# Performance work log

Measured on AMD Instinct MI355X. Metric: run time of the kernel, lower is better.

Reference implementation:

```python
import jax, jax.numpy as jnp
import numpy as np

K = 10
EPS = 1e-5

def leaky(x):
    return jnp.where(x >= 0, x, 0.2 * x)

def graph_feature(x, k):
    # x: (B, C, N) -> edge features (B, 2C, N, k), standard DGCNN get_graph_feature
    B, C, N = x.shape
    xx = jnp.sum(x * x, axis=1)                      # (B, N)
    inner = jnp.einsum('bcn,bcm->bnm', x, x)          # (B, N, N)
    pair = 2.0 * inner - xx[:, :, None] - xx[:, None, :]  # -||xi - xj||^2
    _, idx = jax.lax.top_k(pair, k)                   # (B, N, k)
    xt = jnp.transpose(x, (0, 2, 1))                  # (B, N, C)
    nbr = xt[jnp.arange(B)[:, None, None], idx]       # (B, N, k, C) gather
    ctr = jnp.broadcast_to(xt[:, :, None, :], nbr.shape)
    feat = jnp.concatenate([nbr - ctr, ctr], axis=-1)  # (B, N, k, 2C)
    return jnp.transpose(feat, (0, 3, 1, 2))          # (B, 2C, N, k)

def edge_block(x, W, k):
    # gather -> 1x1 conv (edge MLP) -> leaky relu -> max over neighbors
    e = graph_feature(x, k)                           # (B, 2C, N, k)
    h = leaky(jnp.einsum('oc,bcnk->bonk', W, e))      # (B, O, N, k)
    return jnp.max(h, axis=-1)                        # (B, O, N)

def bn(x, g, b, m, v):
    # inference batchnorm over channel axis 1; x: (B, C, ...) 
    shape = (1, -1) + (1,) * (x.ndim - 2)
    return (x - m.reshape(shape)) * (g.reshape(shape) * jax.lax.rsqrt(v.reshape(shape) + EPS)) + b.reshape(shape)

def setup_inputs() -> dict:
    key = jax.random.key(0)
    ks = jax.random.split(key, 20)
    s = lambda i, shape, scale: (jax.random.normal(ks[i], shape, jnp.float32) * scale)
    inp = {
        'input': jax.random.normal(ks[0], (759, 220, 3), jnp.float32),
        'W1': s(1, (32, 6), 0.4),
        'W2': s(2, (32, 64), 0.15),
        'W3': s(3, (64, 64), 0.15),
        'W4': s(4, (128, 128), 0.1),
        'W5': s(5, (512, 256), 0.08),
        'g5': 1.0 + s(6, (512,), 0.05), 'b5': s(7, (512,), 0.05),
        'm5': s(8, (512,), 0.05), 'v5': 1.0 + 0.1 * jax.random.uniform(ks[9], (512,), jnp.float32),
        'Wl1': s(10, (1024, 1024), 0.03),
        'g6': 1.0 + s(11, (1024,), 0.05), 'b6': s(12, (1024,), 0.05),
        'm6': s(13, (1024,), 0.05), 'v6': 1.0 + 0.1 * jax.random.uniform(ks[14], (1024,), jnp.float32),
        'Wl2': s(15, (380, 1024), 0.03),
        'bl2': s(16, (380,), 0.02),
    }
    return inp

def reference(input, W1, W2, W3, W4, W5, g5, b5, m5, v5, Wl1, g6, b6, m6, v6, Wl2, bl2):
    x = jnp.transpose(input.reshape(-1, 220, 3), (0, 2, 1))  # (B, 3, N)
    x1 = edge_block(x, W1, K)    # (B, 32, N)
    x2 = edge_block(x1, W2, K)   # (B, 32, N)
    x3 = edge_block(x2, W3, K)   # (B, 64, N)
    x4 = edge_block(x3, W4, K)   # (B, 128, N)
    xc = jnp.concatenate([x1, x2, x3, x4], axis=1)           # (B, 256, N)
    h = leaky(bn(jnp.einsum('oc,bcn->bon', W5, xc), g5, b5, m5, v5))  # (B, 512, N)
    p = jnp.concatenate([jnp.max(h, axis=-1), jnp.mean(h, axis=-1)], axis=1)  # (B, 1024)
    z = leaky(bn(p @ Wl1.T, g6, b6, m6, v6))  # dropout is identity in eval
    return z @ Wl2.T + bl2                     # (B, 380)
```

## Files before the change

### kernel.cpp

```cpp
#include <hip/hip_runtime.h>
#include <math.h>

#define NB 759
#define NPT 220
#define KNN 10
#define XCCH 256
#define LDXC (XCCH * NPT)
#define KP 72

typedef float f4 __attribute__((ext_vector_type(4)));
typedef float f16v __attribute__((ext_vector_type(16)));
typedef short bf8v __attribute__((ext_vector_type(8)));
typedef unsigned u4v __attribute__((ext_vector_type(4)));

__device__ inline unsigned short bfh(float x) {
  unsigned u = __float_as_uint(x);
  unsigned r = u + 0x7FFFu + ((u >> 16) & 1u);
  return (unsigned short)(r >> 16);
}
__device__ inline float bff(unsigned short h) {
  return __uint_as_float(((unsigned)h) << 16);
}
__device__ inline void bfsplit(float x, unsigned short& h, unsigned short& l) {
  h = bfh(x);
  l = bfh(x - bff(h));
}

__global__ __launch_bounds__(256) void k_transpose(const float* __restrict__ in, float* __restrict__ x0) {
  int i = blockIdx.x * 256 + threadIdx.x;
  if (i >= NB * 3 * NPT) return;
  int n = i % NPT; int t = i / NPT; int c = t % 3; int b = t / 3;
  x0[i] = in[(b * NPT + n) * 3 + c];
}

__global__ __launch_bounds__(256) void k_w5split(const float* __restrict__ W5,
    unsigned short* __restrict__ Wh, unsigned short* __restrict__ Wl) {
  int i = blockIdx.x * 256 + threadIdx.x;
  if (i >= 512 * 256) return;
  bfsplit(W5[i], Wh[i], Wl[i]);
}

__device__ inline void topk_insert(float d, int m, float* tv, int* ti) {
  if (d > tv[KNN - 1]) {
    tv[KNN - 1] = d; ti[KNN - 1] = m;
    #pragma unroll
    for (int j = KNN - 1; j >= 1; --j) {
      if (tv[j] > tv[j - 1]) {
        float tf = tv[j - 1]; tv[j - 1] = tv[j]; tv[j] = tf;
        int tq = ti[j - 1]; ti[j - 1] = ti[j]; ti[j] = tq;
      } else break;
    }
  }
}

__global__ __launch_bounds__(256) void k_knn3(const float* __restrict__ x, int ldb,
                                              int* __restrict__ idxout) {
  __shared__ __align__(16) float xl[NPT * 4];
  __shared__ float xx[NPT];
  int b = blockIdx.x;
  const float* xb = x + (size_t)b * ldb;
  for (int i = threadIdx.x; i < NPT; i += 256) {
    f4 v; v.x = xb[i]; v.y = xb[NPT + i]; v.z = xb[2 * NPT + i]; v.w = 0.f;
    *(f4*)&xl[i * 4] = v;
    xx[i] = v.x * v.x + v.y * v.y + v.z * v.z;
  }
  __syncthreads();
  int n = threadIdx.x;
  if (n >= NPT) return;
  f4 xn = *(const f4*)&xl[n * 4];
  float xxn = xx[n];
  float tv[KNN]; int ti[KNN];
  #pragma unroll
  for (int k = 0; k < KNN; ++k) { tv[k] = -1e30f; ti[k] = 0; }
  for (int m = 0; m < NPT; ++m) {
    f4 v = *(const f4*)&xl[m * 4];
    float dot = xn.x * v.x + xn.y * v.y + xn.z * v.z;
    topk_insert(2.f * dot - xxn - xx[m], m, tv, ti);
  }
  int* ib = idxout + ((size_t)b * NPT + n) * KNN;
  #pragma unroll
  for (int k = 0; k < KNN; ++k) ib[k] = ti[k];
}

template<int C>
__global__ __launch_bounds__(512) void k_knn_mfma(const float* __restrict__ x, int ldb,
                                                  int* __restrict__ idxout) {
  constexpr int KPG = C + 8;
  constexpr int SW = (C / 16) - 1;
  __shared__ __align__(16) unsigned short XH[224 * KPG];
  __shared__ __align__(16) unsigned short XM[224 * KPG];
  __shared__ __align__(16) unsigned short XL[224 * KPG];
  __shared__ float xx[224];
  int b = blockIdx.x;
  const float* xb = x + (size_t)b * ldb;
  for (int i = threadIdx.x; i < C * 224; i += 512) {
    int c = i / 224, m = i - c * 224;
    float v = (m < NPT) ? xb[c * NPT + m] : 0.f;
    unsigned short h = bfh(v);
    float r1 = v - bff(h);
    unsigned short mm = bfh(r1);
    unsigned short l = bfh(r1 - bff(mm));
    int cs = c ^ ((m & SW) << 4);
    XH[m * KPG + cs] = h; XM[m * KPG + cs] = mm; XL[m * KPG + cs] = l;
  }
  for (int m = threadIdx.x; m < 224; m += 512) {
    float s = 0.f;
    if (m < NPT) {
      for (int c = 0; c < C; ++c) { float v = xb[c * NPT + m]; s += v * v; }
    } else s = 1e30f;
    xx[m] = s;
  }
  __syncthreads();
  int w = threadIdx.x >> 6;
  int lane = threadIdx.x & 63;
  int lc = lane & 31, hi = lane >> 5;
  float tv[KNN]; int ti[KNN];
  #pragma unroll
  for (int k = 0; k < KNN; ++k) { tv[k] = -1e30f; ti[k] = 0; }
  if (w < 7) {
    int n = w * 32 + lc;
    f16v acc[7];
    #pragma unroll
    for (int mt = 0; mt < 7; ++mt)
      #pragma unroll
      for (int i = 0; i < 16; ++i) acc[mt][i] = 0.f;
    #pragma unroll
    for (int ks = 0; ks < C / 16; ++ks) {
      int kb = ks * 16 + hi * 8;
      int nsw = kb ^ ((n & SW) << 4);
      bf8v bh = *(const bf8v*)&XH[n * KPG + nsw];
      bf8v bm = *(const bf8v*)&XM[n * KPG + nsw];
      bf8v bl = *(const bf8v*)&XL[n * KPG + nsw];
      #pragma unroll
      for (int mt = 0; mt < 7; ++mt) {
        int mr = mt * 32 + lc;
        int msw = kb ^ ((mr & SW) << 4);
        bf8v ah = *(const bf8v*)&XH[mr * KPG + msw];
        bf8v am = *(const bf8v*)&XM[mr * KPG + msw];
        bf8v al = *(const bf8v*)&XL[mr * KPG + msw];
        acc[mt] = __builtin_amdgcn_mfma_f32_32x32x16_bf16(ah, bh, acc[mt], 0, 0, 0);
        acc[mt] = __builtin_amdgcn_mfma_f32_32x32x16_bf16(am, bh, acc[mt], 0, 0, 0);
        acc[mt] = __builtin_amdgcn_mfma_f32_32x32x16_bf16(ah, bm, acc[mt], 0, 0, 0);
        acc[mt] = __builtin_amdgcn_mfma_f32_32x32x16_bf16(am, bm, acc[mt], 0, 0, 0);
        acc[mt] = __builtin_amdgcn_mfma_f32_32x32x16_bf16(al, bh, acc[mt], 0, 0, 0);
        acc[mt] = __builtin_amdgcn_mfma_f32_32x32x16_bf16(ah, bl, acc[mt], 0, 0, 0);
      }
    }
    float xxn = xx[n];
    #pragma unroll
    for (int mt = 0; mt < 7; ++mt)
      #pragma unroll
      for (int i = 0; i < 16; ++i) {
        int m = mt * 32 + (i & 3) + 8 * (i >> 2) + 4 * hi;
        float d = 2.f * acc[mt][i] - xx[m] - xxn;
        topk_insert(d, m, tv, ti);
      }
  }
  __syncthreads();
  float* LV = (float*)XH;
  int* LI = (int*)XM;
  if (w < 7) {
    int slot = (w * 64 + lane) * KNN;
    #pragma unroll
    for (int k = 0; k < KNN; ++k) { LV[slot + k] = tv[k]; LI[slot + k] = ti[k]; }
  }
  __syncthreads();
  if (w < 7 && hi == 0) {
    int n = w * 32 + lc;
    if (n < NPT) {
      int sa = (w * 64 + lane) * KNN, sb = sa + 32 * KNN;
      int a = 0, bq = 0;
      int* ob = idxout + ((size_t)b * NPT + n) * KNN;
      #pragma unroll
      for (int k = 0; k < KNN; ++k) {
        float va = LV[sa + a], vb = LV[sb + bq];
        int ia = LI[sa + a], ic = LI[sb + bq];
        bool ta = (va > vb) || (va == vb && ia < ic);
        ob[k] = ta ? ia : ic;
        if (ta) ++a; else ++bq;
      }
    }
  }
}

template<int CIN, int OG, bool WBF16, bool WF32>
__global__ __launch_bounds__(512, 4) void k_conv_fused(const float* __restrict__ x, int ldb,
    const float* __restrict__ W, const int* __restrict__ idxb, float* __restrict__ xout, int ldo,
    unsigned short* __restrict__ xch, unsigned short* __restrict__ xcl, int cbase,
    int csplit, int nch) {
  constexpr int NPAD = 224;
  constexpr int DBS = 225;
  constexpr int REGION = 64 * DBS;
  __shared__ __align__(16) float smem[REGION + CIN * 64];
  __shared__ unsigned short idxl[NPT * KNN];
  float* xl = smem;
  float* db = smem;
  float* wl = smem + REGION;
  int d = blockIdx.x;
  int b, og;
  if (OG == 4)      { b = (d & 7) * 95 + (d >> 5); og = (d >> 3) & 3; }
  else if (OG == 2) { b = (d & 7) * 95 + (d >> 4); og = (d >> 3) & 1; }
  else              { b = d; og = 0; }
  if (b >= NB) return;
  const float* xb = x + (size_t)b * ldb;
  for (int i = threadIdx.x; i < CIN * NPAD; i += 512) {
    int c = i / NPAD, n = i - c * NPAD;
    xl[i] = (n < NPT) ? xb[c * NPT + n] : 0.f;
  }
  for (int i = threadIdx.x; i < 64 * CIN; i += 512) {
    int rl = i & 63, c = i >> 6;
    int o = og * 32 + (rl & 31);
    float wv = (rl < 32) ? W[o * 2 * CIN + c]
                         : (W[o * 2 * CIN + CIN + c] - W[o * 2 * CIN + c]);
    wl[c * 64 + rl] = wv;
  }
  for (int i = threadIdx.x; i < NPT * KNN; i += 512)
    idxl[i] = (unsigned short)idxb[(size_t)b * NPT * KNN + i];
  __syncthreads();
  int rq = threadIdx.x & 15, nq = threadIdx.x >> 4;
  int gv[2]; bool gok[2];
  #pragma unroll
  for (int j = 0; j < 2; ++j) { int g = nq + j * 32; gok[j] = g < 55; gv[j] = (g < 55 ? g : 54) * 4; }
  f4 acc[2][4];
  #pragma unroll
  for (int j = 0; j < 2; ++j)
    #pragma unroll
    for (int i2 = 0; i2 < 4; ++i2) acc[j][i2] = (f4){0.f, 0.f, 0.f, 0.f};
  #pragma unroll 2
  for (int c = 0; c < CIN; ++c) {
    f4 wv = *(const f4*)&wl[c * 64 + rq * 4];
    #pragma unroll
    for (int j = 0; j < 2; ++j) {
      f4 xv = *(const f4*)&xl[c * NPAD + gv[j]];
      acc[j][0] += wv.x * xv; acc[j][1] += wv.y * xv;
      acc[j][2] += wv.z * xv; acc[j][3] += wv.w * xv;
    }
  }
  __syncthreads();
  #pragma unroll
  for (int j = 0; j < 2; ++j) {
    if (gok[j]) {
      #pragma unroll
      for (int i2 = 0; i2 < 4; ++i2) {
        #pragma unroll
        for (int q = 0; q < 4; ++q)
          db[(rq * 4 + i2) * DBS + gv[j] + q] = acc[j][i2][q];
      }
    }
  }
  __syncthreads();
  int o0 = og * 32;
  if (WF32) {
    for (int i = threadIdx.x; i < 32 * NPT; i += 512) {
      int ol = i / NPT, n = i - ol * NPT;
      const float* drow = &db[ol * DBS];
      const unsigned short* ib = &idxl[n * KNN];
      float mx = -1e30f;
      #pragma unroll
      for (int k = 0; k < KNN; ++k) mx = fmaxf(mx, drow[ib[k]]);
      float v = mx + db[(32 + ol) * DBS + n];
      v = (v >= 0.f) ? v : 0.2f * v;
      xout[((size_t)b * ldo + o0 + ol) * NPT + n] = v;
    }
  }
  if (WBF16) {
    for (int i = threadIdx.x; i < 224 * 4; i += 512) {
      int n = i >> 2, cs = i & 3;
      unsigned short hs[8], ls[8];
      if (n < NPT) {
        const unsigned short* ib = &idxl[n * KNN];
        unsigned short ixr[KNN];
        #pragma unroll
        for (int k = 0; k < KNN; ++k) ixr[k] = ib[k];
        #pragma unroll
        for (int j = 0; j < 8; ++j) {
          int ol = cs * 8 + j;
          const float* drow = &db[ol * DBS];
          float mx = -1e30f;
          #pragma unroll
          for (int k = 0; k < KNN; ++k) mx = fmaxf(mx, drow[ixr[k]]);
          float v = mx + db[(32 + ol) * DBS + n];
          v = (v >= 0.f) ? v : 0.2f * v;
          bfsplit(v, hs[j], ls[j]);
        }
      } else {
        #pragma unroll
        for (int j = 0; j < 8; ++j) { hs[j] = 0; ls[j] = 0; }
      }
      int cc0 = cbase + o0 + cs * 8 - csplit;
      size_t off = (((size_t)b * nch + (cc0 >> 6)) * 224 + n) * (size_t)KP + (cc0 & 63);
      u4v hv, lv;
      #pragma unroll
      for (int q = 0; q < 4; ++q) {
        hv[q] = (unsigned)hs[2 * q] | ((unsigned)hs[2 * q + 1] << 16);
        lv[q] = (unsigned)ls[2 * q] | ((unsigned)ls[2 * q + 1] << 16);
      }
      *(u4v*)&xch[off] = hv;
      *(u4v*)&xcl[off] = lv;
    }
  }
}

__global__ __launch_bounds__(256) void k_w5_mfma(const float* __restrict__ xc, int chs,
    const unsigned short* __restrict__ xh, const unsigned short* __restrict__ xlo,
    int split_cb, int nch,
    const unsigned short* __restrict__ Wh, const unsigned short* __restrict__ Wl,
    const float* __restrict__ g5, const float* __restrict__ b5, const float* __restrict__ m5,
    const float* __restrict__ v5, float* __restrict__ p) {
  __shared__ __align__(16) unsigned short XH[224 * KP];
  __shared__ __align__(16) unsigned short XL[224 * KP];
  int d = blockIdx.x;
  int b = (d & 7) * 95 + (d >> 5);
  int rg = (d >> 3) & 3;
  if (b >= NB) return;
  int lane = threadIdx.x & 63, w = threadIdx.x >> 6;
  f16v acc[7];
  #pragma unroll
  for (int t = 0; t < 7; ++t)
    #pragma unroll
    for (int i = 0; i < 16; ++i) acc[t][i] = 0.f;

  int r = rg * 128 + w * 32 + (lane & 31);
  int khalf = (lane >> 5) * 8;

  for (int cb = 0; cb < 4; ++cb) {
    if (cb) __syncthreads();
    if (cb < split_cb) {
      for (int i = threadIdx.x; i < 32 * NPT; i += 256) {
        int cp = i / NPT;
        int n = i - cp * NPT;
        int c0 = cp * 2;
        const float* src = &xc[((size_t)b * chs + cb * 64 + c0) * NPT + n];
        float x0 = src[0];
        float x1 = src[NPT];
        unsigned short h0, l0, h1, l1;
        bfsplit(x0, h0, l0); bfsplit(x1, h1, l1);
        ((unsigned*)XH)[(n * KP + c0) >> 1] = (unsigned)h0 | ((unsigned)h1 << 16);
        ((unsigned*)XL)[(n * KP + c0) >> 1] = (unsigned)l0 | ((unsigned)l1 << 16);
      }
      for (int i = threadIdx.x; i < 4 * 32; i += 256) {
        int n = NPT + (i >> 5); int cd = i & 31;
        ((unsigned*)XH)[n * (KP / 2) + cd] = 0u;
        ((unsigned*)XL)[n * (KP / 2) + cd] = 0u;
      }
    } else {
      int q = cb - split_cb;
      const u4v* sH = (const u4v*)(xh + (((size_t)b * nch + q) * 224) * KP);
      const u4v* sL = (const u4v*)(xlo + (((size_t)b * nch + q) * 224) * KP);
      u4v* dH = (u4v*)XH;
      u4v* dL = (u4v*)XL;
      for (int i = threadIdx.x; i < 224 * KP / 8; i += 256) {
        dH[i] = sH[i];
        dL[i] = sL[i];
      }
    }
    __syncthreads();
    #pragma unroll
    for (int ks = 0; ks < 4; ++ks) {
      int kg = cb * 64 + ks * 16 + khalf;
      int kl = ks * 16 + khalf;
      bf8v ah = *(const bf8v*)&Wh[(size_t)r * 256 + kg];
      bf8v al = *(const bf8v*)&Wl[(size_t)r * 256 + kg];
      #pragma unroll
      for (int t = 0; t < 7; ++t) {
        int col = t * 32 + (lane & 31);
        bf8v bh = *(const bf8v*)&XH[col * KP + kl];
        bf8v bl = *(const bf8v*)&XL[col * KP + kl];
        acc[t] = __builtin_amdgcn_mfma_f32_32x32x16_bf16(ah, bh, acc[t], 0, 0, 0);
        acc[t] = __builtin_amdgcn_mfma_f32_32x32x16_bf16(al, bh, acc[t], 0, 0, 0);
        acc[t] = __builtin_amdgcn_mfma_f32_32x32x16_bf16(ah, bl, acc[t], 0, 0, 0);
      }
    }
  }
  int rbase = rg * 128 + w * 32 + 4 * (lane >> 5);
  int lc = lane & 31;
  #pragma unroll
  for (int i = 0; i < 16; ++i) {
    int row = rbase + (i & 3) + 8 * (i >> 2);
    float a = g5[row] * rsqrtf(v5[row] + 1e-5f);
    float dq = b5[row] - m5[row] * a;
    float mx = -1e30f, sm = 0.f;
    #pragma unroll
    for (int t = 0; t < 7; ++t) {
      bool valid = (t < 6) || (lc < 28);
      float hv = a * acc[t][i] + dq;
      float lv = (hv >= 0.f) ? hv : 0.2f * hv;
      if (valid) { mx = fmaxf(mx, lv); sm += lv; }
    }
    #pragma unroll
    for (int m_ = 1; m_ <= 16; m_ <<= 1) {
      mx = fmaxf(mx, __shfl_xor(mx, m_));
      sm += __shfl_xor(sm, m_);
    }
    if (lc == 0) {
      p[(size_t)b * 1024 + row] = mx;
      p[(size_t)b * 1024 + 512 + row] = sm * (1.f / NPT);
    }
  }
}

template<int ON, bool FUSE>
__global__ __launch_bounds__(256) void k_fc(const float* __restrict__ in, const float* __restrict__ Wt,
    const float* __restrict__ q0, const float* __restrict__ q1, const float* __restrict__ q2,
    const float* __restrict__ q3, float* __restrict__ out, int ostride) {
  __shared__ __align__(16) float il[32 * 68];
  __shared__ __align__(16) float wl[32 * 68];
  int b0 = blockIdx.x * 64, o0 = blockIdx.y * 64;
  int oq = threadIdx.x & 15, bq = threadIdx.x >> 4;
  f4 acc[4];
  #pragma unroll
  for (int i2 = 0; i2 < 4; ++i2) acc[i2] = (f4){0.f, 0.f, 0.f, 0.f};
  for (int cb = 0; cb < 32; ++cb) {
    if (cb) __syncthreads();
    for (int i = threadIdx.x; i < 2048; i += 256) {
      int c = i & 31, bb = i >> 5;
      il[c * 68 + bb] = (b0 + bb < NB) ? in[(b0 + bb) * 1024 + cb * 32 + c] : 0.f;
    }
    for (int i = threadIdx.x; i < 2048; i += 256) {
      int c = i & 31, ol = i >> 5;
      wl[c * 68 + ol] = (o0 + ol < ON) ? Wt[(o0 + ol) * 1024 + cb * 32 + c] : 0.f;
    }
    __syncthreads();
    #pragma unroll
    for (int c = 0; c < 32; ++c) {
      f4 wv = *(const f4*)&wl[c * 68 + oq * 4];
      f4 iv = *(const f4*)&il[c * 68 + bq * 4];
      acc[0] += wv.x * iv; acc[1] += wv.y * iv; acc[2] += wv.z * iv; acc[3] += wv.w * iv;
    }
  }
  #pragma unroll
  for (int i2 = 0; i2 < 4; ++i2) {
    int o = o0 + oq * 4 + i2;
    if (o >= ON) continue;
    float A = 1.f, Dv = 0.f;
    if (FUSE) { float a = q0[o] * rsqrtf(q3[o] + 1e-5f); A = a; Dv = q1[o] - q2[o] * a; }
    else { Dv = q0[o]; }
    #pragma unroll
    for (int jj = 0; jj < 4; ++jj) {
      int bb = b0 + bq * 4 + jj;
      if (bb < NB) {
        float v = acc[i2][jj];
        if (FUSE) { v = A * v + Dv; v = (v >= 0.f) ? v : 0.2f * v; }
        else { v = v + Dv; }
        out[(size_t)bb * ostride + o] = v;
      }
    }
  }
}

extern "C" void kernel_launch(void* const* d_in, const int* in_sizes, int n_in,
                              void* d_out, int out_size, void* d_ws, size_t ws_size,
                              hipStream_t stream) {
  const float* input = (const float*)d_in[0];
  const float* W1 = (const float*)d_in[1];
  const float* W2 = (const float*)d_in[2];
  const float* W3 = (const float*)d_in[3];
  const float* W4 = (const float*)d_in[4];
  const float* W5 = (const float*)d_in[5];
  const float* g5 = (const float*)d_in[6];
  const float* b5 = (const float*)d_in[7];
  const float* m5 = (const float*)d_in[8];
  const float* v5 = (const float*)d_in[9];
  const float* Wl1 = (const float*)d_in[10];
  const float* g6 = (const float*)d_in[11];
  const float* b6 = (const float*)d_in[12];
  const float* m6 = (const float*)d_in[13];
  const float* v6 = (const float*)d_in[14];
  const float* Wl2 = (const float*)d_in[15];
  const float* bl2 = (const float*)d_in[16];

  float* w = (float*)d_ws;
  int NCH = 0;
  if (ws_size >= 4ull * (25229684ull + 12241152ull * 3)) NCH = 3;
  else if (ws_size >= 4ull * (25229684ull + 12241152ull * 2)) NCH = 2;

  float *x0, *xc, *p, *z; int* idxb;
  unsigned short *wh, *wlo, *xh, *xlo;
  int chs, csplit, split_cb;
  if (NCH > 0) {
    x0 = w;
    xc = x0 + 500940;
    p  = xc + 21373440;
    z  = p  + 777216;
    idxb = (int*)(z + 777216);
    wh  = (unsigned short*)(w + 25098612);
    wlo = wh + 131072;
    xh  = wlo + 131072;
    xlo = xh + (size_t)NCH * 12241152;
    chs = 128; csplit = 256 - 64 * NCH; split_cb = 4 - NCH;
  } else {
    x0 = w;
    xc = x0 + 500940;
    p  = xc + 42746880;
    z  = p  + 777216;
    idxb = (int*)(z + 777216);
    wh  = (unsigned short*)(w + 46472052);
    wlo = wh + 131072;
    xh = wlo; xlo = wlo;
    chs = 256; csplit = 256; split_cb = 4;
  }
  int ldxc = chs * NPT;

  k_transpose<<<1957, 256, 0, stream>>>(input, x0);
  k_w5split<<<512, 256, 0, stream>>>(W5, wh, wlo);

  k_knn3<<<759, 256, 0, stream>>>(x0, 3 * NPT, idxb);

  if (NCH == 3) {
    k_conv_fused<3, 1, false, true><<<759, 512, 0, stream>>>(x0, 3 * NPT, W1, idxb, xc, chs, xh, xlo, 0, csplit, NCH);
    k_knn_mfma<32><<<759, 512, 0, stream>>>(xc, ldxc, idxb);
    k_conv_fused<32, 1, false, true><<<759, 512, 0, stream>>>(xc, ldxc, W2, idxb, xc + 32 * NPT, chs, xh, xlo, 32, csplit, NCH);
    k_knn_mfma<32><<<759, 512, 0, stream>>>(xc + 32 * NPT, ldxc, idxb);
    k_conv_fused<32, 2, true, true><<<1520, 512, 0, stream>>>(xc + 32 * NPT, ldxc, W3, idxb, xc + 64 * NPT, chs, xh, xlo, 64, csplit, NCH);
    k_knn_mfma<64><<<759, 512, 0, stream>>>(xc + 64 * NPT, ldxc, idxb);
    k_conv_fused<64, 4, true, false><<<3040, 512, 0, stream>>>(xc + 64 * NPT, ldxc, W4, idxb, xc, 0, xh, xlo, 128, csplit, NCH);
  } else if (NCH == 2) {
    k_conv_fused<3, 1, false, true><<<759, 512, 0, stream>>>(x0, 3 * NPT, W1, idxb, xc, chs, xh, xlo, 0, csplit, NCH);
    k_knn_mfma<32><<<759, 512, 0, stream>>>(xc, ldxc, idxb);
    k_conv_fused<32, 1, false, true><<<759, 512, 0, stream>>>(xc, ldxc, W2, idxb, xc + 32 * NPT, chs, xh, xlo, 32, csplit, NCH);
    k_knn_mfma<32><<<759, 512, 0, stream>>>(xc + 32 * NPT, ldxc, idxb);
    k_conv_fused<32, 2, false, true><<<1520, 512, 0, stream>>>(xc + 32 * NPT, ldxc, W3, idxb, xc + 64 * NPT, chs, xh, xlo, 64, csplit, NCH);
    k_knn_mfma<64><<<759, 512, 0, stream>>>(xc + 64 * NPT, ldxc, idxb);
    k_conv_fused<64, 4, true, false><<<3040, 512, 0, stream>>>(xc + 64 * NPT, ldxc, W4, idxb, xc, 0, xh, xlo, 128, csplit, NCH);
  } else {
    k_conv_fused<3, 1, false, true><<<759, 512, 0, stream>>>(x0, 3 * NPT, W1, idxb, xc, chs, xh, xlo, 0, csplit, NCH);
    k_knn_mfma<32><<<759, 512, 0, stream>>>(xc, ldxc, idxb);
    k_conv_fused<32, 1, false, true><<<759, 512, 0, stream>>>(xc, ldxc, W2, idxb, xc + 32 * NPT, chs, xh, xlo, 32, csplit, NCH);
    k_knn_mfma<32><<<759, 512, 0, stream>>>(xc + 32 * NPT, ldxc, idxb);
    k_conv_fused<32, 2, false, true><<<1520, 512, 0, stream>>>(xc + 32 * NPT, ldxc, W3, idxb, xc + 64 * NPT, chs, xh, xlo, 64, csplit, NCH);
    k_knn_mfma<64><<<759, 512, 0, stream>>>(xc + 64 * NPT, ldxc, idxb);
    k_conv_fused<64, 4, false, true><<<3040, 512, 0, stream>>>(xc + 64 * NPT, ldxc, W4, idxb, xc + 128 * NPT, chs, xh, xlo, 128, csplit, NCH);
  }

  k_w5_mfma<<<3040, 256, 0, stream>>>(xc, chs, xh, xlo, split_cb, NCH, wh, wlo, g5, b5, m5, v5, p);

  k_fc<1024, true><<<dim3(12, 16), 256, 0, stream>>>(p, Wl1, g6, b6, m6, v6, z, 1024);
  k_fc<380, false><<<dim3(12, 6), 256, 0, stream>>>(z, Wl2, bl2, bl2, bl2, bl2, (float*)d_out, 380);
}
```

Measured before the change: 1.499 ms.

## Reorganize bf16 split activation layout into 8-channel groups for W5 MFMA

Changes the staging layout of the bf16 hi/lo activation chunks from a padded row-major [n][72] layout to a grouped [group][n][8] layout, with 32-channel super-chunks. The W5 MFMA kernel now loops over 8 chunks of 32 channels with a smaller LDS footprint and reads B fragments contiguously per group. The intent is to remove LDS padding and bank conflicts, shrink shared memory to raise occupancy, and make the global copy denser. The cost is twice as many barrier-separated load phases in the W5 kernel.

```diff
diff --git a/kernel.cpp b/kernel.cpp
--- a/kernel.cpp
+++ b/kernel.cpp
@@ -187,7 +187,7 @@
 __global__ __launch_bounds__(512, 4) void k_conv_fused(const float* __restrict__ x, int ldb,
     const float* __restrict__ W, const int* __restrict__ idxb, float* __restrict__ xout, int ldo,
     unsigned short* __restrict__ xch, unsigned short* __restrict__ xcl, int cbase,
-    int csplit, int nch) {
+    int csplit, int nsc) {
   constexpr int NPAD = 224;
   constexpr int DBS = 225;
   constexpr int REGION = 64 * DBS;
@@ -287,8 +287,9 @@
         #pragma unroll
         for (int j = 0; j < 8; ++j) { hs[j] = 0; ls[j] = 0; }
       }
-      int cc0 = cbase + o0 + cs * 8 - csplit;
-      size_t off = (((size_t)b * nch + (cc0 >> 6)) * 224 + n) * (size_t)KP + (cc0 & 63);
+      int cc = cbase + o0 + cs * 8 - csplit;
+      int sc = cc >> 5, g = (cc >> 3) & 3;
+      size_t off = ((((size_t)b * nsc + sc) * 4 + g) * 224 + n) * 8;
       u4v hv, lv;
       #pragma unroll
       for (int q = 0; q < 4; ++q) {
@@ -303,12 +304,12 @@
 
 __global__ __launch_bounds__(256) void k_w5_mfma(const float* __restrict__ xc, int chs,
     const unsigned short* __restrict__ xh, const unsigned short* __restrict__ xlo,
-    int split_cb, int nch,
+    int split_sc, int nsc,
     const unsigned short* __restrict__ Wh, const unsigned short* __restrict__ Wl,
     const float* __restrict__ g5, const float* __restrict__ b5, const float* __restrict__ m5,
     const float* __restrict__ v5, float* __restrict__ p) {
-  __shared__ __align__(16) unsigned short XH[224 * KP];
-  __shared__ __align__(16) unsigned short XL[224 * KP];
+  __shared__ __align__(16) unsigned short XH[4 * 224 * 8];
+  __shared__ __align__(16) unsigned short XL[4 * 224 * 8];
   int d = blockIdx.x;
   int b = (d & 7) * 95 + (d >> 5);
   int rg = (d >> 3) & 3;
@@ -322,50 +323,54 @@
 
   int r = rg * 128 + w * 32 + (lane & 31);
   int khalf = (lane >> 5) * 8;
-
-  for (int cb = 0; cb < 4; ++cb) {
-    if (cb) __syncthreads();
-    if (cb < split_cb) {
-      for (int i = threadIdx.x; i < 32 * NPT; i += 256) {
+  unsigned* XHd = (unsigned*)XH;
+  unsigned* XLd = (unsigned*)XL;
+
+  for (int sc = 0; sc < 8; ++sc) {
+    if (sc) __syncthreads();
+    if (sc < split_sc) {
+      for (int i = threadIdx.x; i < 16 * NPT; i += 256) {
         int cp = i / NPT;
         int n = i - cp * NPT;
-        int c0 = cp * 2;
-        const float* src = &xc[((size_t)b * chs + cb * 64 + c0) * NPT + n];
+        int c0 = sc * 32 + cp * 2;
+        const float* src = &xc[((size_t)b * chs + c0) * NPT + n];
         float x0 = src[0];
         float x1 = src[NPT];
         unsigned short h0, l0, h1, l1;
         bfsplit(x0, h0, l0); bfsplit(x1, h1, l1);
-        ((unsigned*)XH)[(n * KP + c0) >> 1] = (unsigned)h0 | ((unsigned)h1 << 16);
-        ((unsigned*)XL)[(n * KP + c0) >> 1] = (unsigned)l0 | ((unsigned)l1 << 16);
-      }
-      for (int i = threadIdx.x; i < 4 * 32; i += 256) {
-        int n = NPT + (i >> 5); int cd = i & 31;
-        ((unsigned*)XH)[n * (KP / 2) + cd] = 0u;
-        ((unsigned*)XL)[n * (KP / 2) + cd] = 0u;
+        int dw = (cp >> 2) * 896 + n * 4 + (cp & 3);
+        XHd[dw] = (unsigned)h0 | ((unsigned)h1 << 16);
+        XLd[dw] = (unsigned)l0 | ((unsigned)l1 << 16);
+      }
+      for (int i = threadIdx.x; i < 64; i += 256) {
+        int g = i >> 4, n = NPT + ((i >> 2) & 3), eh = i & 3;
+        int dw = g * 896 + n * 4 + eh;
+        XHd[dw] = 0u;
+        XLd[dw] = 0u;
       }
     } else {
-      int q = cb - split_cb;
-      const u4v* sH = (const u4v*)(xh + (((size_t)b * nch + q) * 224) * KP);
-      const u4v* sL = (const u4v*)(xlo + (((size_t)b * nch + q) * 224) * KP);
+      int q = sc - split_sc;
+      const u4v* sH = (const u4v*)(xh + ((size_t)b * nsc + q) * 7168);
+      const u4v* sL = (const u4v*)(xlo + ((size_t)b * nsc + q) * 7168);
       u4v* dH = (u4v*)XH;
       u4v* dL = (u4v*)XL;
-      for (int i = threadIdx.x; i < 224 * KP / 8; i += 256) {
+      for (int i = threadIdx.x; i < 896; i += 256) {
         dH[i] = sH[i];
         dL[i] = sL[i];
       }
     }
     __syncthreads();
     #pragma unroll
-    for (int ks = 0; ks < 4; ++ks) {
-      int kg = cb * 64 + ks * 16 + khalf;
-      int kl = ks * 16 + khalf;
+    for (int ks = 0; ks < 2; ++ks) {
+      int kg = sc * 32 + ks * 16 + khalf;
+      int g = ks * 2 + (lane >> 5);
       bf8v ah = *(const bf8v*)&Wh[(size_t)r * 256 + kg];
       bf8v al = *(const bf8v*)&Wl[(size_t)r * 256 + kg];
       #pragma unroll
       for (int t = 0; t < 7; ++t) {
         int col = t * 32 + (lane & 31);
-        bf8v bh = *(const bf8v*)&XH[col * KP + kl];
-        bf8v bl = *(const bf8v*)&XL[col * KP + kl];
+        bf8v bh = *(const bf8v*)&XH[g * 1792 + col * 8];
+        bf8v bl = *(const bf8v*)&XL[g * 1792 + col * 8];
         acc[t] = __builtin_amdgcn_mfma_f32_32x32x16_bf16(ah, bh, acc[t], 0, 0, 0);
         acc[t] = __builtin_amdgcn_mfma_f32_32x32x16_bf16(al, bh, acc[t], 0, 0, 0);
         acc[t] = __builtin_amdgcn_mfma_f32_32x32x16_bf16(ah, bl, acc[t], 0, 0, 0);
@@ -476,7 +481,7 @@
 
   float *x0, *xc, *p, *z; int* idxb;
   unsigned short *wh, *wlo, *xh, *xlo;
-  int chs, csplit, split_cb;
+  int chs, csplit, split_sc, nsc;
   if (NCH > 0) {
     x0 = w;
     xc = x0 + 500940;
@@ -487,7 +492,7 @@
     wlo = wh + 131072;
     xh  = wlo + 131072;
     xlo = xh + (size_t)NCH * 12241152;
-    chs = 128; csplit = 256 - 64 * NCH; split_cb = 4 - NCH;
+    chs = 128; csplit = 256 - 64 * NCH; split_sc = 8 - 2 * NCH; nsc = 2 * NCH;
   } else {
     x0 = w;
     xc = x0 + 500940;
@@ -497,7 +502,7 @@
     wh  = (unsigned short*)(w + 46472052);
     wlo = wh + 131072;
     xh = wlo; xlo = wlo;
-    chs = 256; csplit = 256; split_cb = 4;
+    chs = 256; csplit = 256; split_sc = 8; nsc = 1;
   }
   int ldxc = chs * NPT;
 
@@ -507,32 +512,32 @@
   k_knn3<<<759, 256, 0, stream>>>(x0, 3 * NPT, idxb);
 
   if (NCH == 3) {
-    k_conv_fused<3, 1, false, true><<<759, 512, 0, stream>>>(x0, 3 * NPT, W1, idxb, xc, chs, xh, xlo, 0, csplit, NCH);
+    k_conv_fused<3, 1, false, true><<<759, 512, 0, stream>>>(x0, 3 * NPT, W1, idxb, xc, chs, xh, xlo, 0, csplit, nsc);
     k_knn_mfma<32><<<759, 512, 0, stream>>>(xc, ldxc, idxb);
-    k_conv_fused<32, 1, false, true><<<759, 512, 0, stream>>>(xc, ldxc, W2, idxb, xc + 32 * NPT, chs, xh, xlo, 32, csplit, NCH);
+    k_conv_fused<32, 1, false, true><<<759, 512, 0, stream>>>(xc, ldxc, W2, idxb, xc + 32 * NPT, chs, xh, xlo, 32, csplit, nsc);
     k_knn_mfma<32><<<759, 512, 0, stream>>>(xc + 32 * NPT, ldxc, idxb);
-    k_conv_fused<32, 2, true, true><<<1520, 512, 0, stream>>>(xc + 32 * NPT, ldxc, W3, idxb, xc + 64 * NPT, chs, xh, xlo, 64, csplit, NCH);
+    k_conv_fused<32, 2, true, true><<<1520, 512, 0, stream>>>(xc + 32 * NPT, ldxc, W3, idxb, xc + 64 * NPT, chs, xh, xlo, 64, csplit, nsc);
     k_knn_mfma<64><<<759, 512, 0, stream>>>(xc + 64 * NPT, ldxc, idxb);
-    k_conv_fused<64, 4, true, false><<<3040, 512, 0, stream>>>(xc + 64 * NPT, ldxc, W4, idxb, xc, 0, xh, xlo, 128, csplit, NCH);
+    k_conv_fused<64, 4, true, false><<<3040, 512, 0, stream>>>(xc + 64 * NPT, ldxc, W4, idxb, xc, 0, xh, xlo, 128, csplit, nsc);
   } else if (NCH == 2) {
-    k_conv_fused<3, 1, false, true><<<759, 512, 0, stream>>>(x0, 3 * NPT, W1, idxb, xc, chs, xh, xlo, 0, csplit, NCH);
+    k_conv_fused<3, 1, false, true><<<759, 512, 0, stream>>>(x0, 3 * NPT, W1, idxb, xc, chs, xh, xlo, 0, csplit, nsc);
     k_knn_mfma<32><<<759, 512, 0, stream>>>(xc, ldxc, idxb);
-    k_conv_fused<32, 1, false, true><<<759, 512, 0, stream>>>(xc, ldxc, W2, idxb, xc + 32 * NPT, chs, xh, xlo, 32, csplit, NCH);
+    k_conv_fused<32, 1, false, true><<<759, 512, 0, stream>>>(xc, ldxc, W2, idxb, xc + 32 * NPT, chs, xh, xlo, 32, csplit, nsc);
     k_knn_mfma<32><<<759, 512, 0, stream>>>(xc + 32 * NPT, ldxc, idxb);
-    k_conv_fused<32, 2, false, true><<<1520, 512, 0, stream>>>(xc + 32 * NPT, ldxc, W3, idxb, xc + 64 * NPT, chs, xh, xlo, 64, csplit, NCH);
+    k_conv_fused<32, 2, false, true><<<1520, 512, 0, stream>>>(xc + 32 * NPT, ldxc, W3, idxb, xc + 64 * NPT, chs, xh, xlo, 64, csplit, nsc);
     k_knn_mfma<64><<<759, 512, 0, stream>>>(xc + 64 * NPT, ldxc, idxb);
-    k_conv_fused<64, 4, true, false><<<3040, 512, 0, stream>>>(xc + 64 * NPT, ldxc, W4, idxb, xc, 0, xh, xlo, 128, csplit, NCH);
+    k_conv_fused<64, 4, true, false><<<3040, 512, 0, stream>>>(xc + 64 * NPT, ldxc, W4, idxb, xc, 0, xh, xlo, 128, csplit, nsc);
   } else {
-    k_conv_fused<3, 1, false, true><<<759, 512, 0, stream>>>(x0, 3 * NPT, W1, idxb, xc, chs, xh, xlo, 0, csplit, NCH);
+    k_conv_fused<3, 1, false, true><<<759, 512, 0, stream>>>(x0, 3 * NPT, W1, idxb, xc, chs, xh, xlo, 0, csplit, nsc);
     k_knn_mfma<32><<<759, 512, 0, stream>>>(xc, ldxc, idxb);
-    k_conv_fused<32, 1, false, true><<<759, 512, 0, stream>>>(xc, ldxc, W2, idxb, xc + 32 * NPT, chs, xh, xlo, 32, csplit, NCH);
+    k_conv_fused<32, 1, false, true><<<759, 512, 0, stream>>>(xc, ldxc, W2, idxb, xc + 32 * NPT, chs, xh, xlo, 32, csplit, nsc);
     k_knn_mfma<32><<<759, 512, 0, stream>>>(xc + 32 * NPT, ldxc, idxb);
-    k_conv_fused<32, 2, false, true><<<1520, 512, 0, stream>>>(xc + 32 * NPT, ldxc, W3, idxb, xc + 64 * NPT, chs, xh, xlo, 64, csplit, NCH);
+    k_conv_fused<32, 2, false, true><<<1520, 512, 0, stream>>>(xc + 32 * NPT, ldxc, W3, idxb, xc + 64 * NPT, chs, xh, xlo, 64, csplit, nsc);
     k_knn_mfma<64><<<759, 512, 0, stream>>>(xc + 64 * NPT, ldxc, idxb);
-    k_conv_fused<64, 4, false, true><<<3040, 512, 0, stream>>>(xc + 64 * NPT, ldxc, W4, idxb, xc + 128 * NPT, chs, xh, xlo, 128, csplit, NCH);
-  }
-
-  k_w5_mfma<<<3040, 256, 0, stream>>>(xc, chs, xh, xlo, split_cb, NCH, wh, wlo, g5, b5, m5, v5, p);
+    k_conv_fused<64, 4, false, true><<<3040, 512, 0, stream>>>(xc + 64 * NPT, ldxc, W4, idxb, xc + 128 * NPT, chs, xh, xlo, 128, csplit, nsc);
+  }
+
+  k_w5_mfma<<<3040, 256, 0, stream>>>(xc, chs, xh, xlo, split_sc, nsc, wh, wlo, g5, b5, m5, v5, p);
 
   k_fc<1024, true><<<dim3(12, 16), 256, 0, stream>>>(p, Wl1, g6, b6, m6, v6, z, 1024);
   k_fc<380, false><<<dim3(12, 6), 256, 0, stream>>>(z, Wl2, bl2, bl2, bl2, bl2, (float*)d_out, 380);
```

Measured after the change: 1.528 ms. About the same (+1.9%).
